# Kernel tuning notes

Hardware: AMD Instinct MI355X
Metric: run time of the kernel (lower is better)

## Reference

```python
import jax, jax.numpy as jnp
import numpy as np

N = 50000      # batch_node_num (unique nodes)
E = 800000     # number of edges (avg degree 16)
IN = 128       # in_dim
OUT = 128      # out_dim
B = 10000      # query nodes


def setup_inputs() -> dict:
    key = jax.random.key(0)
    k = jax.random.split(key, 8)
    edges = jax.random.randint(k[0], (E, 2), 0, N, dtype=jnp.int64)
    node_idx = jax.random.randint(k[1], (B,), 0, N, dtype=jnp.int64)
    local_features = jax.random.normal(k[2], (N, IN), dtype=jnp.float32)
    W1 = jax.random.normal(k[3], (IN, OUT), dtype=jnp.float32) * (1.0 / np.sqrt(IN))
    b1 = jnp.zeros((OUT,), dtype=jnp.float32)
    W2 = jax.random.normal(k[4], (OUT, OUT), dtype=jnp.float32) * (1.0 / np.sqrt(OUT))
    b2 = jnp.zeros((OUT,), dtype=jnp.float32)
    return {"edges": edges, "node_idx": node_idx, "local_features": local_features,
            "W1": W1, "b1": b1, "W2": W2, "b2": b2, "ind": 2}


def reference(edges, node_idx, local_features, W1, b1, W2, b2, ind):
    mask = jnp.array([1.0, 1.0, 0.0, 0.0], dtype=jnp.float32)
    # Linear -> Tanh -> Linear (the out_linear_layer MLP)
    h = jnp.tanh(local_features @ W1 + b1) @ W2 + b2          # [N, OUT]
    src, dst = edges[:, 0], edges[:, 1]
    # self-loop edges get weight mask[ind], others weight 1
    values = jnp.where(src == dst, mask[ind], jnp.float32(1.0))  # [E]
    # spmm(matrix, ones) == per-row degree (weighted)
    row_sum = jax.ops.segment_sum(values, src, num_segments=N)   # [N]
    row_sum = jnp.where(row_sum == 0, jnp.float32(1.0), row_sum)
    # spmm(matrix, new_embeddings): gather dst embeddings, scatter-add to src
    results = jax.ops.segment_sum(values[:, None] * h[dst], src, num_segments=N)  # [N, OUT]
    output_emb = results / row_sum[:, None]
    return output_emb[node_idx]
```

## Files before the change

### kernel.cpp

```cpp
#include <hip/hip_runtime.h>

#define IN_DIM 128
#define CAP 128
#define LDT 136
#define SCAT_BLOCKS 384

typedef short v8s __attribute__((ext_vector_type(8)));
typedef float v4f __attribute__((ext_vector_type(4)));

__device__ inline unsigned short f2bf(float f) {
    unsigned int u = __float_as_uint(f);
    u += 0x7FFFu + ((u >> 16) & 1u);
    return (unsigned short)(u >> 16);
}
__device__ inline float bf2f(unsigned short h) {
    return __uint_as_float((unsigned int)h << 16);
}

__global__ __launch_bounds__(256) void prep(
    const float* __restrict__ W1, const float* __restrict__ W2,
    unsigned short* __restrict__ Wt1, unsigned short* __restrict__ Wt2,
    const int* __restrict__ node_idx, int* __restrict__ flag, int B,
    int* __restrict__ cursor, int N, int nbF)
{
    int bid = blockIdx.x;
    if (bid < 128) {
        int i = bid * 256 + threadIdx.x;
        int m = i >> 14, rem = i & 16383;
        int n = rem >> 7, k = rem & 127;
        float wv = (m ? W2 : W1)[k * 128 + n];
        (m ? Wt2 : Wt1)[n * 128 + k] = f2bf(wv);
    } else if (bid < 128 + nbF) {
        int i = (bid - 128) * 256 + threadIdx.x;
        if (i < B) flag[node_idx[i]] = 1;
    } else {
        int i = (bid - 128 - nbF) * 256 + threadIdx.x;
        if (i < N) cursor[i] = 0;
    }
}

__global__ __launch_bounds__(256, 1) void mlp_fill(
    const float* __restrict__ X,
    const unsigned short* __restrict__ Wt1, const unsigned short* __restrict__ Wt2,
    const float* __restrict__ b1, const float* __restrict__ b2,
    unsigned short* __restrict__ Hb, int nrows,
    const int* __restrict__ edges, const int* __restrict__ flag,
    const int* __restrict__ indp, int* __restrict__ cursor,
    unsigned short* __restrict__ col, int E, int mlpBlocks)
{
    __shared__ unsigned short Ts[4 * 32 * LDT];
    const int bid = blockIdx.x;

    if (bid >= mlpBlocks) {
        const int keepSelf = (*indp < 2) ? 1 : 0;
        const int stride = SCAT_BLOCKS * 256;
        for (int e = (bid - mlpBlocks) * 256 + threadIdx.x; e < E; e += stride) {
            int2 ed = ((const int2*)edges)[e];
            if ((ed.x != ed.y || keepSelf) && flag[ed.x] == 1) {
                int p = atomicAdd(&cursor[ed.x], 1);
                if (p < CAP)
                    col[(size_t)ed.x * CAP + p] = (unsigned short)ed.y;
            }
        }
        return;
    }

    const int t    = threadIdx.x;
    const int w    = t >> 6;
    const int lane = t & 63;
    const int l15  = lane & 15;
    const int quad = lane >> 4;
    const int R0   = bid * 128;
    const int wrow = w * 32;
    unsigned short* Tw = &Ts[w * 32 * LDT];

    int gr0 = R0 + wrow + l15;        gr0 = gr0 < nrows ? gr0 : nrows - 1;
    int gr1 = R0 + wrow + 16 + l15;   gr1 = gr1 < nrows ? gr1 : nrows - 1;
    const float* xrow[2] = { &X[(size_t)gr0 * 128 + quad * 8],
                             &X[(size_t)gr1 * 128 + quad * 8] };

    v4f acc[2][8];
#pragma unroll
    for (int rt = 0; rt < 2; ++rt)
#pragma unroll
        for (int ct = 0; ct < 8; ++ct)
            acc[rt][ct] = (v4f){0.f, 0.f, 0.f, 0.f};

#pragma unroll
    for (int h = 0; h < 2; ++h) {
        v8s Bf[2][8];
#pragma unroll
        for (int kq = 0; kq < 2; ++kq) {
            const int kk = h * 2 + kq;
#pragma unroll
            for (int ct = 0; ct < 8; ++ct)
                Bf[kq][ct] = *(const v8s*)
                    &Wt1[(size_t)(ct * 16 + l15) * 128 + kk * 32 + quad * 8];
        }
        v8s Ar[2][2];
#pragma unroll
        for (int kq = 0; kq < 2; ++kq) {
            const int kk = h * 2 + kq;
#pragma unroll
            for (int rt = 0; rt < 2; ++rt) {
                const float* xp = xrow[rt] + kk * 32;
                float4 x0 = *(const float4*)xp;
                float4 x1 = *(const float4*)(xp + 4);
                v8s av;
                av[0] = (short)f2bf(x0.x); av[1] = (short)f2bf(x0.y);
                av[2] = (short)f2bf(x0.z); av[3] = (short)f2bf(x0.w);
                av[4] = (short)f2bf(x1.x); av[5] = (short)f2bf(x1.y);
                av[6] = (short)f2bf(x1.z); av[7] = (short)f2bf(x1.w);
                Ar[kq][rt] = av;
            }
        }
#pragma unroll
        for (int kq = 0; kq < 2; ++kq)
#pragma unroll
            for (int ct = 0; ct < 8; ++ct)
#pragma unroll
                for (int rt = 0; rt < 2; ++rt)
                    acc[rt][ct] = __builtin_amdgcn_mfma_f32_16x16x32_bf16(
                        Ar[kq][rt], Bf[kq][ct], acc[rt][ct], 0, 0, 0);
    }
#pragma unroll
    for (int ct = 0; ct < 8; ++ct) {
        float bias = b1[ct * 16 + l15];
#pragma unroll
        for (int rt = 0; rt < 2; ++rt) {
#pragma unroll
            for (int r = 0; r < 4; ++r)
                Tw[(rt * 16 + quad * 4 + r) * LDT + ct * 16 + l15] =
                    f2bf(tanhf(acc[rt][ct][r] + bias));
            acc[rt][ct] = (v4f){0.f, 0.f, 0.f, 0.f};
        }
    }
    asm volatile("s_waitcnt lgkmcnt(0)" ::: "memory");

#pragma unroll
    for (int h = 0; h < 2; ++h) {
        v8s Bf[2][8];
#pragma unroll
        for (int kq = 0; kq < 2; ++kq) {
            const int kk = h * 2 + kq;
#pragma unroll
            for (int ct = 0; ct < 8; ++ct)
                Bf[kq][ct] = *(const v8s*)
                    &Wt2[(size_t)(ct * 16 + l15) * 128 + kk * 32 + quad * 8];
        }
        v8s Ar[2][2];
#pragma unroll
        for (int kq = 0; kq < 2; ++kq) {
            const int kk = h * 2 + kq;
#pragma unroll
            for (int rt = 0; rt < 2; ++rt)
                Ar[kq][rt] = *(const v8s*)
                    &Tw[(rt * 16 + l15) * LDT + kk * 32 + quad * 8];
        }
#pragma unroll
        for (int kq = 0; kq < 2; ++kq)
#pragma unroll
            for (int ct = 0; ct < 8; ++ct)
#pragma unroll
                for (int rt = 0; rt < 2; ++rt)
                    acc[rt][ct] = __builtin_amdgcn_mfma_f32_16x16x32_bf16(
                        Ar[kq][rt], Bf[kq][ct], acc[rt][ct], 0, 0, 0);
    }
    asm volatile("s_waitcnt lgkmcnt(0)" ::: "memory");
#pragma unroll
    for (int ct = 0; ct < 8; ++ct) {
        float bias = b2[ct * 16 + l15];
#pragma unroll
        for (int rt = 0; rt < 2; ++rt)
#pragma unroll
            for (int r = 0; r < 4; ++r)
                Tw[(rt * 16 + quad * 4 + r) * LDT + ct * 16 + l15] =
                    f2bf(acc[rt][ct][r] + bias);
    }
    asm volatile("s_waitcnt lgkmcnt(0)" ::: "memory");
#pragma unroll
    for (int i = 0; i < 8; ++i) {
        int lr = i * 4 + quad;
        int c  = l15;
        uint4 v = *(const uint4*)&Tw[lr * LDT + c * 8];
        int grow = R0 + wrow + lr;
        if (grow < nrows)
            *(uint4*)&Hb[(size_t)grow * 128 + c * 8] = v;
    }
}

__global__ __launch_bounds__(256) void aggregate_out(
    const int* __restrict__ node_idx, const int* __restrict__ cursor,
    const unsigned short* __restrict__ col, const unsigned short* __restrict__ Hb,
    float* __restrict__ out, int B)
{
    int b = (int)((blockIdx.x * blockDim.x + threadIdx.x) >> 6);
    if (b >= B) return;
    int lane = threadIdx.x & 63;
    int v = node_idx[b];
    int deg = cursor[v];
    deg = deg < CAP ? deg : CAP;
    const unsigned short* cp = &col[(size_t)v * CAP];
    int myc = (lane < deg) ? (int)cp[lane] : 0;
    int dmax = deg < 64 ? deg : 64;
    float ax = 0.f, ay = 0.f, bx = 0.f, by = 0.f;
    int i = 0;
    for (; i + 1 < dmax; i += 2) {
        int d0 = __shfl(myc, i, 64);
        int d1 = __shfl(myc, i + 1, 64);
        unsigned int u0 = *(const unsigned int*)&Hb[(size_t)d0 * 128 + lane * 2];
        unsigned int u1 = *(const unsigned int*)&Hb[(size_t)d1 * 128 + lane * 2];
        ax += bf2f((unsigned short)(u0 & 0xFFFFu));
        ay += bf2f((unsigned short)(u0 >> 16));
        bx += bf2f((unsigned short)(u1 & 0xFFFFu));
        by += bf2f((unsigned short)(u1 >> 16));
    }
    if (i < dmax) {
        int d0 = __shfl(myc, i, 64);
        unsigned int u0 = *(const unsigned int*)&Hb[(size_t)d0 * 128 + lane * 2];
        ax += bf2f((unsigned short)(u0 & 0xFFFFu));
        ay += bf2f((unsigned short)(u0 >> 16));
    }
    for (int j = 64; j < deg; ++j) {
        int d0 = cp[j];
        unsigned int u0 = *(const unsigned int*)&Hb[(size_t)d0 * 128 + lane * 2];
        ax += bf2f((unsigned short)(u0 & 0xFFFFu));
        ay += bf2f((unsigned short)(u0 >> 16));
    }
    float den = (deg > 0) ? (float)deg : 1.0f;
    *(float2*)&out[(size_t)b * 128 + lane * 2] =
        make_float2((ax + bx) / den, (ay + by) / den);
}

extern "C" void kernel_launch(void* const* d_in, const int* in_sizes, int n_in,
                              void* d_out, int out_size, void* d_ws, size_t ws_size,
                              hipStream_t stream)
{
    const int*   edges    = (const int*)d_in[0];
    const int*   node_idx = (const int*)d_in[1];
    const float* X        = (const float*)d_in[2];
    const float* W1       = (const float*)d_in[3];
    const float* b1       = (const float*)d_in[4];
    const float* W2       = (const float*)d_in[5];
    const float* b2       = (const float*)d_in[6];
    const int*   indp     = (const int*)d_in[7];

    const int E = in_sizes[0] / 2;
    const int B = in_sizes[1];
    const int N = in_sizes[2] / IN_DIM;
    const int mlpBlocks = (N + 127) / 128;
    const int nbF = (B + 255) / 256;
    const int nbC = (N + 255) / 256;

    char* ws = (char*)d_ws;
    size_t off = 0;
    int* cursor = (int*)(ws + off); off += (size_t)N * 4;
    int* flag   = (int*)(ws + off); off += (size_t)N * 4;
    off = (off + 15) & ~(size_t)15;
    unsigned short* Hb  = (unsigned short*)(ws + off); off += (size_t)N * IN_DIM * 2;
    unsigned short* col = (unsigned short*)(ws + off); off += (size_t)N * CAP * 2;
    unsigned short* Wt1 = (unsigned short*)(ws + off); off += 16384 * 2;
    unsigned short* Wt2 = (unsigned short*)(ws + off); off += 16384 * 2;

    hipLaunchKernelGGL(prep, dim3(128 + nbF + nbC), dim3(256), 0, stream,
                       W1, W2, Wt1, Wt2, node_idx, flag, B, cursor, N, nbF);
    hipLaunchKernelGGL(mlp_fill, dim3(mlpBlocks + SCAT_BLOCKS), dim3(256),
                       0, stream, X, Wt1, Wt2, b1, b2, Hb, N,
                       edges, flag, indp, cursor, col, E, mlpBlocks);
    hipLaunchKernelGGL(aggregate_out, dim3((B * 64 + 255) / 256), dim3(256), 0,
                       stream, node_idx, cursor, col, Hb, (float*)d_out, B);
}
```

Before: 129.4 us.

## Stage XOR-swizzled bf16 weights in LDS and raise occupancy to two blocks

The transposed bf16 weights are now written with an XOR swizzle on 8-element chunks. Each MLP block copies W1 (then W2) into a 32 KB shared buffer and reads its B fragments from LDS, where the swizzle is meant to avoid bank conflicts, instead of from global memory. The k-loop now handles one 32-wide k-slice at a time, which lowers register pressure, and launch bounds allow two blocks per CU. In exchange it adds a global-to-LDS copy and extra __syncthreads per block, plus more shared memory per block, which could limit the occupancy gain.

```diff
diff --git a/kernel.cpp b/kernel.cpp
--- a/kernel.cpp
+++ b/kernel.cpp
@@ -29,7 +29,8 @@
         int m = i >> 14, rem = i & 16383;
         int n = rem >> 7, k = rem & 127;
         float wv = (m ? W2 : W1)[k * 128 + n];
-        (m ? Wt2 : Wt1)[n * 128 + k] = f2bf(wv);
+        int idx = n * 128 + (((k >> 3) ^ (n & 15)) << 3) + (k & 7);
+        (m ? Wt2 : Wt1)[idx] = f2bf(wv);
     } else if (bid < 128 + nbF) {
         int i = (bid - 128) * 256 + threadIdx.x;
         if (i < B) flag[node_idx[i]] = 1;
@@ -39,7 +40,7 @@
     }
 }
 
-__global__ __launch_bounds__(256, 1) void mlp_fill(
+__global__ __launch_bounds__(256, 2) void mlp_fill(
     const float* __restrict__ X,
     const unsigned short* __restrict__ Wt1, const unsigned short* __restrict__ Wt2,
     const float* __restrict__ b1, const float* __restrict__ b2,
@@ -48,7 +49,6 @@
     const int* __restrict__ indp, int* __restrict__ cursor,
     unsigned short* __restrict__ col, int E, int mlpBlocks)
 {
-    __shared__ unsigned short Ts[4 * 32 * LDT];
     const int bid = blockIdx.x;
 
     if (bid >= mlpBlocks) {
@@ -65,6 +65,9 @@
         return;
     }
 
+    __shared__ uint4 Wl4[2048];
+    __shared__ unsigned short Ts[4 * 32 * LDT];
+    const unsigned short* Wls = (const unsigned short*)Wl4;
     const int t    = threadIdx.x;
     const int w    = t >> 6;
     const int lane = t & 63;
@@ -79,6 +82,10 @@
     const float* xrow[2] = { &X[(size_t)gr0 * 128 + quad * 8],
                              &X[(size_t)gr1 * 128 + quad * 8] };
 
+#pragma unroll
+    for (int j = 0; j < 8; ++j)
+        Wl4[j * 256 + t] = ((const uint4*)Wt1)[j * 256 + t];
+
     v4f acc[2][8];
 #pragma unroll
     for (int rt = 0; rt < 2; ++rt)
@@ -86,42 +93,34 @@
         for (int ct = 0; ct < 8; ++ct)
             acc[rt][ct] = (v4f){0.f, 0.f, 0.f, 0.f};
 
-#pragma unroll
-    for (int h = 0; h < 2; ++h) {
-        v8s Bf[2][8];
-#pragma unroll
-        for (int kq = 0; kq < 2; ++kq) {
-            const int kk = h * 2 + kq;
-#pragma unroll
-            for (int ct = 0; ct < 8; ++ct)
-                Bf[kq][ct] = *(const v8s*)
-                    &Wt1[(size_t)(ct * 16 + l15) * 128 + kk * 32 + quad * 8];
+    __syncthreads();
+
+#pragma unroll
+    for (int kk = 0; kk < 4; ++kk) {
+        v8s Bf[8];
+#pragma unroll
+        for (int ct = 0; ct < 8; ++ct)
+            Bf[ct] = *(const v8s*)
+                &Wls[(ct * 16 + l15) * 128 + (((kk * 4 + quad) ^ l15) * 8)];
+        v8s Ar[2];
+#pragma unroll
+        for (int rt = 0; rt < 2; ++rt) {
+            const float* xp = xrow[rt] + kk * 32;
+            float4 x0 = *(const float4*)xp;
+            float4 x1 = *(const float4*)(xp + 4);
+            v8s av;
+            av[0] = (short)f2bf(x0.x); av[1] = (short)f2bf(x0.y);
+            av[2] = (short)f2bf(x0.z); av[3] = (short)f2bf(x0.w);
+            av[4] = (short)f2bf(x1.x); av[5] = (short)f2bf(x1.y);
+            av[6] = (short)f2bf(x1.z); av[7] = (short)f2bf(x1.w);
+            Ar[rt] = av;
         }
-        v8s Ar[2][2];
-#pragma unroll
-        for (int kq = 0; kq < 2; ++kq) {
-            const int kk = h * 2 + kq;
-#pragma unroll
-            for (int rt = 0; rt < 2; ++rt) {
-                const float* xp = xrow[rt] + kk * 32;
-                float4 x0 = *(const float4*)xp;
-                float4 x1 = *(const float4*)(xp + 4);
-                v8s av;
-                av[0] = (short)f2bf(x0.x); av[1] = (short)f2bf(x0.y);
-                av[2] = (short)f2bf(x0.z); av[3] = (short)f2bf(x0.w);
-                av[4] = (short)f2bf(x1.x); av[5] = (short)f2bf(x1.y);
-                av[6] = (short)f2bf(x1.z); av[7] = (short)f2bf(x1.w);
-                Ar[kq][rt] = av;
-            }
-        }
-#pragma unroll
-        for (int kq = 0; kq < 2; ++kq)
-#pragma unroll
-            for (int ct = 0; ct < 8; ++ct)
-#pragma unroll
-                for (int rt = 0; rt < 2; ++rt)
-                    acc[rt][ct] = __builtin_amdgcn_mfma_f32_16x16x32_bf16(
-                        Ar[kq][rt], Bf[kq][ct], acc[rt][ct], 0, 0, 0);
+#pragma unroll
+        for (int ct = 0; ct < 8; ++ct)
+#pragma unroll
+            for (int rt = 0; rt < 2; ++rt)
+                acc[rt][ct] = __builtin_amdgcn_mfma_f32_16x16x32_bf16(
+                    Ar[rt], Bf[ct], acc[rt][ct], 0, 0, 0);
     }
 #pragma unroll
     for (int ct = 0; ct < 8; ++ct) {
@@ -135,36 +134,31 @@
             acc[rt][ct] = (v4f){0.f, 0.f, 0.f, 0.f};
         }
     }
-    asm volatile("s_waitcnt lgkmcnt(0)" ::: "memory");
-
-#pragma unroll
-    for (int h = 0; h < 2; ++h) {
-        v8s Bf[2][8];
-#pragma unroll
-        for (int kq = 0; kq < 2; ++kq) {
-            const int kk = h * 2 + kq;
-#pragma unroll
-            for (int ct = 0; ct < 8; ++ct)
-                Bf[kq][ct] = *(const v8s*)
-                    &Wt2[(size_t)(ct * 16 + l15) * 128 + kk * 32 + quad * 8];
-        }
-        v8s Ar[2][2];
-#pragma unroll
-        for (int kq = 0; kq < 2; ++kq) {
-            const int kk = h * 2 + kq;
+
+    __syncthreads();
+#pragma unroll
+    for (int j = 0; j < 8; ++j)
+        Wl4[j * 256 + t] = ((const uint4*)Wt2)[j * 256 + t];
+    __syncthreads();
+
+#pragma unroll
+    for (int kk = 0; kk < 4; ++kk) {
+        v8s Bf[8];
+#pragma unroll
+        for (int ct = 0; ct < 8; ++ct)
+            Bf[ct] = *(const v8s*)
+                &Wls[(ct * 16 + l15) * 128 + (((kk * 4 + quad) ^ l15) * 8)];
+        v8s Ar[2];
+#pragma unroll
+        for (int rt = 0; rt < 2; ++rt)
+            Ar[rt] = *(const v8s*)
+                &Tw[(rt * 16 + l15) * LDT + kk * 32 + quad * 8];
+#pragma unroll
+        for (int ct = 0; ct < 8; ++ct)
 #pragma unroll
             for (int rt = 0; rt < 2; ++rt)
-                Ar[kq][rt] = *(const v8s*)
-                    &Tw[(rt * 16 + l15) * LDT + kk * 32 + quad * 8];
-        }
-#pragma unroll
-        for (int kq = 0; kq < 2; ++kq)
-#pragma unroll
-            for (int ct = 0; ct < 8; ++ct)
-#pragma unroll
-                for (int rt = 0; rt < 2; ++rt)
-                    acc[rt][ct] = __builtin_amdgcn_mfma_f32_16x16x32_bf16(
-                        Ar[kq][rt], Bf[kq][ct], acc[rt][ct], 0, 0, 0);
+                acc[rt][ct] = __builtin_amdgcn_mfma_f32_16x16x32_bf16(
+                    Ar[rt], Bf[ct], acc[rt][ct], 0, 0, 0);
     }
     asm volatile("s_waitcnt lgkmcnt(0)" ::: "memory");
 #pragma unroll
```

Result: faster. 122.8 us, median of 2 (-5.1%).
